# Kernel tuning notes

Hardware: AMD Instinct MI355X
Metric: run time of the kernel (lower is better)

## Reference

```python
import jax, jax.numpy as jnp
import numpy as np

LN_EPS = 1e-5


def _layer_norm(x, scale, bias):
    mu = jnp.mean(x, axis=-1, keepdims=True)
    var = jnp.mean(jnp.square(x - mu), axis=-1, keepdims=True)
    return (x - mu) * jax.lax.rsqrt(var + LN_EPS) * scale + bias


def setup_inputs() -> dict:
    key = jax.random.key(0)
    B, N, C_Z, C_H = 1, 512, 128, 128
    ks = jax.random.split(key, 8)
    s = 1.0 / np.sqrt(C_Z)
    inp = {
        "z": jax.random.normal(ks[0], (B, N, N, C_Z), dtype=jnp.float32),
        "mask": jnp.ones((B, N, N), dtype=jnp.float32),
        # gated / plain projections from c_z -> c_hidden
        "w_a_p": jax.random.normal(ks[1], (C_Z, C_H), dtype=jnp.float32) * s,
        "b_a_p": jnp.zeros((C_H,), dtype=jnp.float32),
        "w_a_g": jnp.zeros((C_Z, C_H), dtype=jnp.float32),  # gating init: zeros, bias ones
        "b_a_g": jnp.ones((C_H,), dtype=jnp.float32),
        "w_b_p": jax.random.normal(ks[2], (C_Z, C_H), dtype=jnp.float32) * s,
        "b_b_p": jnp.zeros((C_H,), dtype=jnp.float32),
        "w_b_g": jnp.zeros((C_Z, C_H), dtype=jnp.float32),
        "b_b_g": jnp.ones((C_H,), dtype=jnp.float32),
        # output gate c_z -> c_z (gating init)
        "w_g": jnp.zeros((C_Z, C_Z), dtype=jnp.float32),
        "b_g": jnp.ones((C_Z,), dtype=jnp.float32),
        # final projection c_hidden -> c_z ('final' init: zeros; use small randn for a nontrivial test)
        "w_z": jax.random.normal(ks[3], (C_H, C_Z), dtype=jnp.float32) * (1.0 / np.sqrt(C_H)),
        "b_z": jnp.zeros((C_Z,), dtype=jnp.float32),
        "ln_in_scale": jnp.ones((C_Z,), dtype=jnp.float32),
        "ln_in_bias": jnp.zeros((C_Z,), dtype=jnp.float32),
        "ln_out_scale": jnp.ones((C_H,), dtype=jnp.float32),
        "ln_out_bias": jnp.zeros((C_H,), dtype=jnp.float32),
    }
    return inp


def reference(z, mask, w_a_p, b_a_p, w_a_g, b_a_g, w_b_p, b_b_p, w_b_g, b_b_g,
              w_g, b_g, w_z, b_z, ln_in_scale, ln_in_bias, ln_out_scale, ln_out_bias):
    # tmu_type == 'outgoing'
    z = _layer_norm(z, ln_in_scale, ln_in_bias)          # [B,N,N,Cz]
    m = mask[..., None]                                   # [B,N,N,1]
    a = jax.nn.sigmoid(z @ w_a_g + b_a_g) * m * (z @ w_a_p + b_a_p)  # [B,N,N,Ch]
    b = jax.nn.sigmoid(z @ w_b_g + b_b_g) * m * (z @ w_b_p + b_b_p)  # [B,N,N,Ch]
    # outgoing: p[b,i,j,c] = sum_k a[b,i,k,c] * b[b,j,k,c]
    x = jnp.einsum("bikc,bjkc->bijc", a, b)              # [B,N,N,Ch]
    x = _layer_norm(x, ln_out_scale, ln_out_bias)
    x = x @ w_z + b_z                                    # [B,N,N,Cz]
    g = jax.nn.sigmoid(z @ w_g + b_g)                    # [B,N,N,Cz]
    return x * g
```

## Files before the change

kernel.cpp:

```cpp
#include <hip/hip_runtime.h>

typedef __attribute__((ext_vector_type(8))) short short8;
typedef __attribute__((ext_vector_type(4))) short short4v;
typedef __attribute__((ext_vector_type(4))) float float4v;
typedef __attribute__((ext_vector_type(2))) unsigned int uint2v;

#define NDIM 512
#define NN (NDIM*NDIM)
#define CD 128

__device__ __forceinline__ unsigned short f2b(float f) {
  union { float f; unsigned u; } v; v.f = f;
  unsigned r = v.u + 0x7FFFu + ((v.u >> 16) & 1u);
  return (unsigned short)(r >> 16);
}
__device__ __forceinline__ float b2f(unsigned short h) {
  union { unsigned u; float f; } v; v.u = ((unsigned)h) << 16; return v.f;
}
__device__ __forceinline__ float sigmoidf_(float x) { return 1.f / (1.f + __expf(-x)); }
__device__ __forceinline__ unsigned pk2(float a, float b) {
  unsigned r;
  asm("v_cvt_pk_bf16_f32 %0, %1, %2" : "=v"(r) : "v"(a), "v"(b));
  return r;
}
__device__ __forceinline__ float4v mfma16(short8 a, short8 b, float4v c) {
  return __builtin_amdgcn_mfma_f32_16x16x32_bf16(a, b, c, 0, 0, 0);
}
__device__ __forceinline__ void gl_lds16(const short* g, short* l) {
  __builtin_amdgcn_global_load_lds(
      (const __attribute__((address_space(1))) unsigned int*)g,
      (__attribute__((address_space(3))) unsigned int*)l, 16, 0, 0);
}

__device__ __forceinline__ short8 fragr(const short* buf, int row, int j) {
  return *(const short8*)(buf + row * 128 + ((j ^ (row & 15)) << 3));
}

__global__ __launch_bounds__(256) void kPrepW(
    const float* __restrict__ w0, const float* __restrict__ w1,
    const float* __restrict__ w2, const float* __restrict__ w3,
    const float* __restrict__ w4, short* __restrict__ wt)
{
  const int wi = blockIdx.y;
  const float* W = wi==0 ? w0 : wi==1 ? w1 : wi==2 ? w2 : wi==3 ? w3 : w4;
  const int e = blockIdx.x * 256 + threadIdx.x;
  const int k = e >> 7, n = e & 127;
  wt[wi * 16384 + n * 128 + k] = (short)f2b(W[k * CD + n]);
}

__global__ __launch_bounds__(256, 2) void kProj(
    const float* __restrict__ z, const float* __restrict__ mask,
    const short* __restrict__ wT,
    const float* __restrict__ b_a_p, const float* __restrict__ b_a_g,
    const float* __restrict__ b_b_p, const float* __restrict__ b_b_g,
    const float* __restrict__ b_g,
    const float* __restrict__ ln_s, const float* __restrict__ ln_b,
    short* __restrict__ a_t, short* __restrict__ b_t, short* __restrict__ g_out)
{
  __shared__ short zln[128 * 128];
  __shared__ short sW[128 * 128];
  const int t = threadIdx.x;
  const int r0 = blockIdx.x * 128;
  const int w = t >> 6, l = t & 63, lr = l & 15, lg = l >> 4;

  int soff[8], doff[8];
#pragma unroll
  for (int i = 0; i < 8; ++i) {
    int U = i * 256 + t;
    int row = U >> 4, u = U & 15;
    soff[i] = row * 128 + ((u ^ (row & 15)) << 3);
    doff[i] = U * 8;
  }
#define STAGE(BUF, SLOT) do { _Pragma("unroll") for (int i_ = 0; i_ < 8; ++i_) \
    gl_lds16(wT + (SLOT) * 16384 + soff[i_], (BUF) + doff[i_]); } while(0)

  STAGE(sW, 1);

#pragma unroll
  for (int h = 0; h < 2; ++h) {
    const int row = h * 64 + (t >> 2), q = t & 3;
    const float* zp = z + (size_t)(r0 + row) * CD + q * 32;
    float x[32];
#pragma unroll
    for (int i = 0; i < 8; ++i) {
      float4v v = *(const float4v*)(zp + i * 4);
#pragma unroll
      for (int e = 0; e < 4; ++e) x[i*4+e] = v[e];
    }
    float s = 0.f;
#pragma unroll
    for (int i = 0; i < 32; ++i) s += x[i];
    s += __shfl_xor(s, 1, 64);
    s += __shfl_xor(s, 2, 64);
    const float mu = s * (1.f/128.f);
    float vs = 0.f;
#pragma unroll
    for (int i = 0; i < 32; ++i) { float d = x[i]-mu; vs += d*d; }
    vs += __shfl_xor(vs, 1, 64);
    vs += __shfl_xor(vs, 2, 64);
    const float rstd = rsqrtf(vs * (1.f/128.f) + 1e-5f);
#pragma unroll
    for (int i = 0; i < 32; i += 2) {
      int c = q*32 + i;
      float y0 = (x[i]  -mu)*rstd*ln_s[c]   + ln_b[c];
      float y1 = (x[i+1]-mu)*rstd*ln_s[c+1] + ln_b[c+1];
      int addr = row*128 + (((c>>3) ^ (row & 15)) << 3) + (c & 7);
      *(unsigned*)(&zln[addr]) = pk2(y0, y1);
    }
  }

  float bga[8], bpa[8], bgb[8], bpb[8];
#pragma unroll
  for (int cf = 0; cf < 8; ++cf) {
    bga[cf] = b_a_g[cf*16+lr]; bpa[cf] = b_a_p[cf*16+lr];
    bgb[cf] = b_b_g[cf*16+lr]; bpb[cf] = b_b_p[cf*16+lr];
  }
  float mrow[2][4];
#pragma unroll
  for (int g = 0; g < 2; ++g)
#pragma unroll
    for (int jj = 0; jj < 4; ++jj)
      mrow[g][jj] = mask[r0 + w*32 + g*16 + lg*4 + jj];

  __syncthreads();

  short8 af[2][4];
#pragma unroll
  for (int g = 0; g < 2; ++g)
#pragma unroll
    for (int ks = 0; ks < 4; ++ks)
      af[g][ks] = fragr(zln, w*32 + g*16 + lr, ks*4 + lg);
  __syncthreads();

  float4v accA[2][8], accB[2][8];
  float sg[2][8][4];

#define ZERO_ACC(A) do { _Pragma("unroll") for (int g_=0;g_<2;++g_) \
  _Pragma("unroll") for (int c_=0;c_<8;++c_) A[g_][c_] = (float4v){0.f,0.f,0.f,0.f}; } while(0)

#define WPASS(A, BUF) do { ZERO_ACC(A);                                    \
  __builtin_amdgcn_s_setprio(1);                                           \
  _Pragma("unroll") for (int ks_=0; ks_<4; ++ks_)                          \
    _Pragma("unroll") for (int cf_=0; cf_<8; ++cf_) {                      \
      short8 wf_ = fragr(BUF, cf_*16 + lr, ks_*4 + lg);                    \
      _Pragma("unroll") for (int g_=0; g_<2; ++g_)                         \
        A[g_][cf_] = mfma16(af[g_][ks_], wf_, A[g_][cf_]);                 \
    }                                                                      \
  __builtin_amdgcn_s_setprio(0); } while(0)

#define SIGPASS(BG) do { _Pragma("unroll") for (int g_=0;g_<2;++g_)        \
  _Pragma("unroll") for (int cf_=0;cf_<8;++cf_)                            \
    _Pragma("unroll") for (int j_=0;j_<4;++j_)                             \
      sg[g_][cf_][j_] = sigmoidf_(accA[g_][cf_][j_] + BG[cf_]) * mrow[g_][j_]; } while(0)

#define STORE_AB(DST, BP) do { _Pragma("unroll") for (int g_=0;g_<2;++g_)  \
  _Pragma("unroll") for (int cf_=0;cf_<8;++cf_) {                          \
    float v0_ = sg[g_][cf_][0] * (accB[g_][cf_][0] + BP[cf_]);             \
    float v1_ = sg[g_][cf_][1] * (accB[g_][cf_][1] + BP[cf_]);             \
    float v2_ = sg[g_][cf_][2] * (accB[g_][cf_][2] + BP[cf_]);             \
    float v3_ = sg[g_][cf_][3] * (accB[g_][cf_][3] + BP[cf_]);             \
    uint2v pv_ = { pk2(v0_, v1_), pk2(v2_, v3_) };                         \
    *(uint2v*)(DST + (size_t)(cf_*16+lr)*NN + r0 + w*32 + g_*16 + lg*4) = pv_; \
  } } while(0)

  STAGE(zln, 0);
  WPASS(accA, sW);
  __syncthreads();
  STAGE(sW, 3);
  WPASS(accB, zln);
  SIGPASS(bga);
  __syncthreads();
  STAGE(zln, 2);
  WPASS(accA, sW);
  STORE_AB(a_t, bpa);
  __syncthreads();
  STAGE(sW, 4);
  WPASS(accB, zln);
  SIGPASS(bgb);
  __syncthreads();

  {
    float4v accG[2][8];
    ZERO_ACC(accG);
    __builtin_amdgcn_s_setprio(1);
#pragma unroll
    for (int ks = 0; ks < 4; ++ks)
#pragma unroll
      for (int cf = 0; cf < 8; ++cf) {
        short8 wf = fragr(sW, cf*16 + lr, ks*4 + lg);
#pragma unroll
        for (int g = 0; g < 2; ++g)
          accG[g][cf] = mfma16(wf, af[g][ks], accG[g][cf]);
      }
    __builtin_amdgcn_s_setprio(0);
    STORE_AB(b_t, bpb);
#pragma unroll
    for (int g = 0; g < 2; ++g)
#pragma unroll
      for (int cf = 0; cf < 8; ++cf) {
        float4v bgv = *(const float4v*)(b_g + cf*16 + lg*4);
        float v0 = sigmoidf_(accG[g][cf][0] + bgv[0]);
        float v1 = sigmoidf_(accG[g][cf][1] + bgv[1]);
        float v2 = sigmoidf_(accG[g][cf][2] + bgv[2]);
        float v3 = sigmoidf_(accG[g][cf][3] + bgv[3]);
        uint2v pv = { pk2(v0, v1), pk2(v2, v3) };
        *(uint2v*)(g_out + (size_t)(r0 + w*32 + g*16 + lr)*CD + cf*16 + lg*4) = pv;
      }
  }
}

__global__ __launch_bounds__(256, 2) void kEinsum(const short* __restrict__ a_t,
                                                  const short* __restrict__ b_t,
                                                  short* __restrict__ x_t)
{
  __shared__ short As[2][128 * 64];
  __shared__ short Bs[2][128 * 64];
  const int t = threadIdx.x;
  const int d = blockIdx.x;
  const int c = (d & 7) * 16 + (d >> 7);
  const int tile = (d >> 3) & 15;
  const int i0 = (tile >> 2) * 128;
  const int j0 = (tile & 3) * 128;
  const size_t abase = (size_t)c * NN;
  const int w = t >> 6, l = t & 63, lr = l & 15, lg = l >> 4;
  const int wr = w >> 1, wc = w & 1;

  const short* gA[4]; const short* gB[4]; int ldsU[4];
#pragma unroll
  for (int q = 0; q < 4; ++q) {
    int U = q * 256 + t;
    int row = U >> 3, u = U & 7;
    int swz = ((u ^ (row & 7)) << 3);
    gA[q] = a_t + abase + (size_t)(i0 + row) * NDIM + swz;
    gB[q] = b_t + abase + (size_t)(j0 + row) * NDIM + swz;
    ldsU[q] = U * 8;
  }

#define STAGE_E(buf, k0) do { _Pragma("unroll") for (int q_=0;q_<4;++q_) { \
    gl_lds16(gA[q_] + (k0), &As[buf][ldsU[q_]]);                           \
    gl_lds16(gB[q_] + (k0), &Bs[buf][ldsU[q_]]); } } while(0)

  float4v acc[4][4];
#pragma unroll
  for (int m = 0; m < 4; ++m)
#pragma unroll
    for (int n = 0; n < 4; ++n) acc[m][n] = (float4v){0.f,0.f,0.f,0.f};

  STAGE_E(0, 0);
  __syncthreads();
  int cur = 0;
#pragma unroll
  for (int it = 0; it < 8; ++it) {
    if (it < 7) STAGE_E(cur ^ 1, (it + 1) * 64);
    short8 afr[4][2], bfr[4][2];
#pragma unroll
    for (int m = 0; m < 4; ++m)
#pragma unroll
      for (int ks = 0; ks < 2; ++ks) {
        int row = wr*64 + m*16 + lr, j = ks*4 + lg;
        afr[m][ks] = *(const short8*)(&As[cur][row*64 + ((j ^ (row & 7)) << 3)]);
      }
#pragma unroll
    for (int n = 0; n < 4; ++n)
#pragma unroll
      for (int ks = 0; ks < 2; ++ks) {
        int row = wc*64 + n*16 + lr, j = ks*4 + lg;
        bfr[n][ks] = *(const short8*)(&Bs[cur][row*64 + ((j ^ (row & 7)) << 3)]);
      }
    __builtin_amdgcn_s_setprio(1);
#pragma unroll
    for (int ks = 0; ks < 2; ++ks)
#pragma unroll
      for (int m = 0; m < 4; ++m)
#pragma unroll
        for (int n = 0; n < 4; ++n)
          acc[m][n] = mfma16(bfr[n][ks], afr[m][ks], acc[m][n]);
    __builtin_amdgcn_s_setprio(0);
    __syncthreads();
    cur ^= 1;
  }
#pragma unroll
  for (int m = 0; m < 4; ++m)
#pragma unroll
    for (int n = 0; n < 4; ++n) {
      int i  = i0 + wr*64 + m*16 + lr;
      int jb = j0 + wc*64 + n*16 + lg*4;
      uint2v pv = { pk2(acc[m][n][0], acc[m][n][1]), pk2(acc[m][n][2], acc[m][n][3]) };
      *(uint2v*)(x_t + abase + (size_t)i * NDIM + jb) = pv;
    }
}

__global__ __launch_bounds__(256, 2) void kOut(
    const short* __restrict__ x_t, const short* __restrict__ g_in,
    const float* __restrict__ w_z, const float* __restrict__ b_z,
    const float* __restrict__ ln_s, const float* __restrict__ ln_b,
    float* __restrict__ out)
{
  __shared__ short xs[128 * 72];
  __shared__ short xln[64 * 128];
  __shared__ short sW[128 * 128];
  const int t = threadIdx.x;
  const int r0 = blockIdx.x * 64;
  const int w = t >> 6, l = t & 63, lr = l & 15, lg = l >> 4;

#pragma unroll
  for (int i = 0; i < 8; ++i) {
    int flat = i * 256 + t;
    int kp = flat >> 5, k = kp * 2, n4 = (flat & 31) * 4;
    float4v va = *(const float4v*)(w_z + (size_t)k * CD + n4);
    float4v vb = *(const float4v*)(w_z + (size_t)(k + 1) * CD + n4);
#pragma unroll
    for (int j = 0; j < 4; ++j) {
      int row = n4 + j;
      int addr = row * 128 + (((k >> 3) ^ (row & 15)) << 3) + (k & 7);
      *(unsigned*)(&sW[addr]) = pk2(va[j], vb[j]);
    }
  }
#pragma unroll
  for (int it = 0; it < 4; ++it) {
    int v = it * 256 + t; int cc = v >> 3; int u = v & 7;
    int up = u ^ ((cc >> 3) & 7);
    *(short8*)&xs[cc * 72 + up * 8] = *(const short8*)(x_t + (size_t)cc * NN + r0 + u * 8);
  }
  __syncthreads();
  {
    const int r = t >> 2, q = t & 3;
    float x[32];
#pragma unroll
    for (int i = 0; i < 32; ++i) {
      int c = q * 32 + i;
      x[i] = b2f((unsigned short)xs[c * 72 + (((r >> 3) ^ ((c >> 3) & 7)) << 3) + (r & 7)]);
    }
    float s = 0.f;
#pragma unroll
    for (int i = 0; i < 32; ++i) s += x[i];
    s += __shfl_xor(s, 1, 64);
    s += __shfl_xor(s, 2, 64);
    const float mu = s * (1.f/128.f);
    float vs = 0.f;
#pragma unroll
    for (int i = 0; i < 32; ++i) { float d = x[i]-mu; vs += d*d; }
    vs += __shfl_xor(vs, 1, 64);
    vs += __shfl_xor(vs, 2, 64);
    const float rstd = rsqrtf(vs * (1.f/128.f) + 1e-5f);
#pragma unroll
    for (int i = 0; i < 32; ++i) {
      int c = q*32 + i;
      float y = (x[i]-mu)*rstd*ln_s[c] + ln_b[c];
      xln[r*128 + (((c>>3) ^ (r & 15)) << 3) + (c & 7)] = (short)f2b(y);
    }
  }
  __syncthreads();
  short8 af[4];
#pragma unroll
  for (int ks = 0; ks < 4; ++ks)
    af[ks] = fragr(xln, w*16 + lr, ks*4 + lg);

  float4v acc[8];
#pragma unroll
  for (int cf = 0; cf < 8; ++cf) acc[cf] = (float4v){0.f,0.f,0.f,0.f};
#pragma unroll
  for (int ks = 0; ks < 4; ++ks)
#pragma unroll
    for (int cf = 0; cf < 8; ++cf) {
      short8 wf = fragr(sW, cf*16 + lr, ks*4 + lg);
      acc[cf] = mfma16(wf, af[ks], acc[cf]);
    }
  const int orow = r0 + w*16 + lr;
#pragma unroll
  for (int cf = 0; cf < 8; ++cf) {
    float4v bzv = *(const float4v*)(b_z + cf*16 + lg*4);
    short4v gv = *(const short4v*)(g_in + (size_t)orow * CD + cf*16 + lg*4);
    float4v o;
#pragma unroll
    for (int j = 0; j < 4; ++j)
      o[j] = (acc[cf][j] + bzv[j]) * b2f((unsigned short)gv[j]);
    *(float4v*)(out + (size_t)orow * CD + cf*16 + lg*4) = o;
  }
}

extern "C" void kernel_launch(void* const* d_in, const int* in_sizes, int n_in,
                              void* d_out, int out_size, void* d_ws, size_t ws_size,
                              hipStream_t stream) {
  (void)in_sizes; (void)n_in; (void)out_size; (void)ws_size;
  const float* z     = (const float*)d_in[0];
  const float* mask  = (const float*)d_in[1];
  const float* w_a_p = (const float*)d_in[2];
  const float* b_a_p = (const float*)d_in[3];
  const float* w_a_g = (const float*)d_in[4];
  const float* b_a_g = (const float*)d_in[5];
  const float* w_b_p = (const float*)d_in[6];
  const float* b_b_p = (const float*)d_in[7];
  const float* w_b_g = (const float*)d_in[8];
  const float* b_b_g = (const float*)d_in[9];
  const float* w_g   = (const float*)d_in[10];
  const float* b_g   = (const float*)d_in[11];
  const float* w_z   = (const float*)d_in[12];
  const float* b_z   = (const float*)d_in[13];
  const float* ln_i_s = (const float*)d_in[14];
  const float* ln_i_b = (const float*)d_in[15];
  const float* ln_o_s = (const float*)d_in[16];
  const float* ln_o_b = (const float*)d_in[17];

  short* a_t = (short*)d_ws;
  short* b_t = a_t + (size_t)CD*NN;
  short* g_s = b_t + (size_t)CD*NN;
  short* x_t = g_s + (size_t)CD*NN;
  short* wT  = x_t;

  hipLaunchKernelGGL(kPrepW, dim3(64, 5), dim3(256), 0, stream,
                     w_a_p, w_a_g, w_b_p, w_b_g, w_g, wT);
  hipLaunchKernelGGL(kProj, dim3(NN/128), dim3(256), 0, stream,
                     z, mask, wT, b_a_p, b_a_g, b_b_p, b_b_g, b_g,
                     ln_i_s, ln_i_b, a_t, b_t, g_s);
  hipLaunchKernelGGL(kEinsum, dim3(2048), dim3(256), 0, stream, a_t, b_t, x_t);
  hipLaunchKernelGGL(kOut, dim3(NN/64), dim3(256), 0, stream,
                     x_t, g_s, w_z, b_z, ln_o_s, ln_o_b, (float*)d_out);
}
```

Baseline: 369.4 us.

## Stage epilogue outputs through LDS for coalesced 16-byte global stores

All three kernels (projection, einsum, output) now write their results into swizzled shared-memory buffers first, then issue contiguous 16-byte vector stores to global memory. Before, each thread did scattered 8-byte stores. The projection kernel's pass order is reshuffled so a extra staging buffer and register-held halves can hold the a/b/g outputs while the MFMA passes run. This aims to cut uncoalesced write traffic, at the cost of extra LDS use, more barriers, and higher register pressure that may reduce occupancy.

Measured after the change: 347.9 us. 5.8% less time.

```diff
diff --git a/kernel.cpp b/kernel.cpp
--- a/kernel.cpp
+++ b/kernel.cpp
@@ -3,7 +3,6 @@
 typedef __attribute__((ext_vector_type(8))) short short8;
 typedef __attribute__((ext_vector_type(4))) short short4v;
 typedef __attribute__((ext_vector_type(4))) float float4v;
-typedef __attribute__((ext_vector_type(2))) unsigned int uint2v;
 
 #define NDIM 512
 #define NN (NDIM*NDIM)
@@ -34,6 +33,9 @@
 
 __device__ __forceinline__ short8 fragr(const short* buf, int row, int j) {
   return *(const short8*)(buf + row * 128 + ((j ^ (row & 15)) << 3));
+}
+__device__ __forceinline__ void stg_w(short* buf, int row, int ku, unsigned v) {
+  *(unsigned*)&buf[row * 128 + ((((ku >> 2) ^ (row & 15)) << 3) + ((ku & 3) << 1))] = v;
 }
 
 __global__ __launch_bounds__(256) void kPrepW(
@@ -59,6 +61,7 @@
 {
   __shared__ short zln[128 * 128];
   __shared__ short sW[128 * 128];
+  __shared__ short sStage[64 * 128];
   const int t = threadIdx.x;
   const int r0 = blockIdx.x * 128;
   const int w = t >> 6, l = t & 63, lr = l & 15, lg = l >> 4;
@@ -132,8 +135,9 @@
       af[g][ks] = fragr(zln, w*32 + g*16 + lr, ks*4 + lg);
   __syncthreads();
 
-  float4v accA[2][8], accB[2][8];
+  float4v accG[2][8], accB[2][8];
   float sg[2][8][4];
+  unsigned avh2[16], bvp[32];
 
 #define ZERO_ACC(A) do { _Pragma("unroll") for (int g_=0;g_<2;++g_) \
   _Pragma("unroll") for (int c_=0;c_<8;++c_) A[g_][c_] = (float4v){0.f,0.f,0.f,0.f}; } while(0)
@@ -151,61 +155,109 @@
 #define SIGPASS(BG) do { _Pragma("unroll") for (int g_=0;g_<2;++g_)        \
   _Pragma("unroll") for (int cf_=0;cf_<8;++cf_)                            \
     _Pragma("unroll") for (int j_=0;j_<4;++j_)                             \
-      sg[g_][cf_][j_] = sigmoidf_(accA[g_][cf_][j_] + BG[cf_]) * mrow[g_][j_]; } while(0)
-
-#define STORE_AB(DST, BP) do { _Pragma("unroll") for (int g_=0;g_<2;++g_)  \
-  _Pragma("unroll") for (int cf_=0;cf_<8;++cf_) {                          \
-    float v0_ = sg[g_][cf_][0] * (accB[g_][cf_][0] + BP[cf_]);             \
-    float v1_ = sg[g_][cf_][1] * (accB[g_][cf_][1] + BP[cf_]);             \
-    float v2_ = sg[g_][cf_][2] * (accB[g_][cf_][2] + BP[cf_]);             \
-    float v3_ = sg[g_][cf_][3] * (accB[g_][cf_][3] + BP[cf_]);             \
-    uint2v pv_ = { pk2(v0_, v1_), pk2(v2_, v3_) };                         \
-    *(uint2v*)(DST + (size_t)(cf_*16+lr)*NN + r0 + w*32 + g_*16 + lg*4) = pv_; \
-  } } while(0)
+      sg[g_][cf_][j_] = sigmoidf_(accG[g_][cf_][j_] + BG[cf_]) * mrow[g_][j_]; } while(0)
 
   STAGE(zln, 0);
-  WPASS(accA, sW);
+  WPASS(accG, sW);
+  SIGPASS(bga);
   __syncthreads();
   STAGE(sW, 3);
   WPASS(accB, zln);
-  SIGPASS(bga);
+#pragma unroll
+  for (int g = 0; g < 2; ++g)
+#pragma unroll
+    for (int cf = 0; cf < 8; ++cf) {
+      float v0 = sg[g][cf][0]*(accB[g][cf][0]+bpa[cf]);
+      float v1 = sg[g][cf][1]*(accB[g][cf][1]+bpa[cf]);
+      float v2 = sg[g][cf][2]*(accB[g][cf][2]+bpa[cf]);
+      float v3 = sg[g][cf][3]*(accB[g][cf][3]+bpa[cf]);
+      unsigned p0 = pk2(v0,v1), p1 = pk2(v2,v3);
+      int ku = w*16 + g*8 + lg*2;
+      if (cf < 4) { stg_w(sStage, cf*16+lr, ku, p0); stg_w(sStage, cf*16+lr, ku+1, p1); }
+      else { avh2[g*8+(cf-4)*2] = p0; avh2[g*8+(cf-4)*2+1] = p1; }
+    }
   __syncthreads();
   STAGE(zln, 2);
-  WPASS(accA, sW);
-  STORE_AB(a_t, bpa);
+  WPASS(accG, sW);
+  SIGPASS(bgb);
+#pragma unroll
+  for (int i = 0; i < 4; ++i) {
+    int ch = t >> 2, cL = (t & 3)*4 + i;
+    *(short8*)(a_t + (size_t)ch*NN + r0 + cL*8) = fragr(sStage, ch, cL);
+  }
   __syncthreads();
   STAGE(sW, 4);
+#pragma unroll
+  for (int g = 0; g < 2; ++g)
+#pragma unroll
+    for (int cf = 0; cf < 4; ++cf) {
+      int ku = w*16 + g*8 + lg*2;
+      stg_w(sStage, cf*16+lr, ku,   avh2[g*8+cf*2]);
+      stg_w(sStage, cf*16+lr, ku+1, avh2[g*8+cf*2+1]);
+    }
   WPASS(accB, zln);
-  SIGPASS(bgb);
-  __syncthreads();
-
-  {
-    float4v accG[2][8];
-    ZERO_ACC(accG);
-    __builtin_amdgcn_s_setprio(1);
-#pragma unroll
-    for (int ks = 0; ks < 4; ++ks)
-#pragma unroll
-      for (int cf = 0; cf < 8; ++cf) {
-        short8 wf = fragr(sW, cf*16 + lr, ks*4 + lg);
-#pragma unroll
-        for (int g = 0; g < 2; ++g)
-          accG[g][cf] = mfma16(wf, af[g][ks], accG[g][cf]);
-      }
-    __builtin_amdgcn_s_setprio(0);
-    STORE_AB(b_t, bpb);
-#pragma unroll
-    for (int g = 0; g < 2; ++g)
-#pragma unroll
-      for (int cf = 0; cf < 8; ++cf) {
-        float4v bgv = *(const float4v*)(b_g + cf*16 + lg*4);
-        float v0 = sigmoidf_(accG[g][cf][0] + bgv[0]);
-        float v1 = sigmoidf_(accG[g][cf][1] + bgv[1]);
-        float v2 = sigmoidf_(accG[g][cf][2] + bgv[2]);
-        float v3 = sigmoidf_(accG[g][cf][3] + bgv[3]);
-        uint2v pv = { pk2(v0, v1), pk2(v2, v3) };
-        *(uint2v*)(g_out + (size_t)(r0 + w*32 + g*16 + lr)*CD + cf*16 + lg*4) = pv;
-      }
+#pragma unroll
+  for (int g = 0; g < 2; ++g)
+#pragma unroll
+    for (int cf = 0; cf < 8; ++cf) {
+      float v0 = sg[g][cf][0]*(accB[g][cf][0]+bpb[cf]);
+      float v1 = sg[g][cf][1]*(accB[g][cf][1]+bpb[cf]);
+      float v2 = sg[g][cf][2]*(accB[g][cf][2]+bpb[cf]);
+      float v3 = sg[g][cf][3]*(accB[g][cf][3]+bpb[cf]);
+      bvp[g*16+cf*2]   = pk2(v0,v1);
+      bvp[g*16+cf*2+1] = pk2(v2,v3);
+    }
+  __syncthreads();
+  float4v accG2[2][8];
+  ZERO_ACC(accG2);
+  __builtin_amdgcn_s_setprio(1);
+#pragma unroll
+  for (int ks = 0; ks < 4; ++ks)
+#pragma unroll
+    for (int cf = 0; cf < 8; ++cf) {
+      short8 wf = fragr(sW, cf*16 + lr, ks*4 + lg);
+#pragma unroll
+      for (int g = 0; g < 2; ++g)
+        accG2[g][cf] = mfma16(wf, af[g][ks], accG2[g][cf]);
+    }
+  __builtin_amdgcn_s_setprio(0);
+#pragma unroll
+  for (int i = 0; i < 4; ++i) {
+    int ch = t >> 2, cL = (t & 3)*4 + i;
+    *(short8*)(a_t + (size_t)(64 + ch)*NN + r0 + cL*8) = fragr(sStage, ch, cL);
+  }
+  __syncthreads();
+#pragma unroll
+  for (int g = 0; g < 2; ++g)
+#pragma unroll
+    for (int cf = 0; cf < 8; ++cf) {
+      int ku = w*16 + g*8 + lg*2;
+      stg_w(zln, cf*16+lr, ku,   bvp[g*16+cf*2]);
+      stg_w(zln, cf*16+lr, ku+1, bvp[g*16+cf*2+1]);
+    }
+#pragma unroll
+  for (int g = 0; g < 2; ++g)
+#pragma unroll
+    for (int cf = 0; cf < 8; ++cf) {
+      float4v bgv = *(const float4v*)(b_g + cf*16 + lg*4);
+      float v0 = sigmoidf_(accG2[g][cf][0] + bgv[0]);
+      float v1 = sigmoidf_(accG2[g][cf][1] + bgv[1]);
+      float v2 = sigmoidf_(accG2[g][cf][2] + bgv[2]);
+      float v3 = sigmoidf_(accG2[g][cf][3] + bgv[3]);
+      int row = w*32 + g*16 + lr, ku = cf*8 + lg*2;
+      stg_w(sW, row, ku,   pk2(v0,v1));
+      stg_w(sW, row, ku+1, pk2(v2,v3));
+    }
+  __syncthreads();
+#pragma unroll
+  for (int i = 0; i < 8; ++i) {
+    int ch = t >> 1, cL = (t & 1)*8 + i;
+    *(short8*)(b_t + (size_t)ch*NN + r0 + cL*8) = fragr(zln, ch, cL);
+  }
+#pragma unroll
+  for (int i = 0; i < 8; ++i) {
+    int row = t >> 1, cL = (t & 1)*8 + i;
+    *(short8*)(g_out + (size_t)(r0 + row)*CD + cL*8) = fragr(sW, row, cL);
   }
 }
 
@@ -279,15 +331,22 @@
     __syncthreads();
     cur ^= 1;
   }
+  short* Xs = &As[0][0];
 #pragma unroll
   for (int m = 0; m < 4; ++m)
 #pragma unroll
     for (int n = 0; n < 4; ++n) {
-      int i  = i0 + wr*64 + m*16 + lr;
-      int jb = j0 + wc*64 + n*16 + lg*4;
-      uint2v pv = { pk2(acc[m][n][0], acc[m][n][1]), pk2(acc[m][n][2], acc[m][n][3]) };
-      *(uint2v*)(x_t + abase + (size_t)i * NDIM + jb) = pv;
-    }
+      int il = wr*64 + m*16 + lr;
+      int ku = wc*32 + n*8 + lg*2;
+      stg_w(Xs, il, ku,   pk2(acc[m][n][0], acc[m][n][1]));
+      stg_w(Xs, il, ku+1, pk2(acc[m][n][2], acc[m][n][3]));
+    }
+  __syncthreads();
+#pragma unroll
+  for (int i = 0; i < 8; ++i) {
+    int il = t >> 1, cL = (t & 1)*8 + i;
+    *(short8*)(x_t + abase + (size_t)(i0 + il)*NDIM + j0 + cL*8) = fragr(Xs, il, cL);
+  }
 }
 
 __global__ __launch_bounds__(256, 2) void kOut(
@@ -366,7 +425,10 @@
       short8 wf = fragr(sW, cf*16 + lr, ks*4 + lg);
       acc[cf] = mfma16(wf, af[ks], acc[cf]);
     }
+  __syncthreads();
+  float* fWs = (float*)sW;
   const int orow = r0 + w*16 + lr;
+  const int rl = w*16 + lr;
 #pragma unroll
   for (int cf = 0; cf < 8; ++cf) {
     float4v bzv = *(const float4v*)(b_z + cf*16 + lg*4);
@@ -375,7 +437,14 @@
 #pragma unroll
     for (int j = 0; j < 4; ++j)
       o[j] = (acc[cf][j] + bzv[j]) * b2f((unsigned short)gv[j]);
-    *(float4v*)(out + (size_t)orow * CD + cf*16 + lg*4) = o;
+    *(float4v*)&fWs[rl*128 + (((cf*4+lg) ^ (rl & 15)) << 2)] = o;
+  }
+  __syncthreads();
+#pragma unroll
+  for (int i = 0; i < 8; ++i) {
+    int row = t >> 2, cL = (t & 3)*8 + i;
+    *(float4v*)(out + (size_t)(r0 + row)*CD + cL*4) =
+        *(const float4v*)&fWs[row*128 + ((cL ^ (row & 15)) << 2)];
   }
 }
 
```
